# Kernel tuning notes

Hardware: AMD Instinct MI355X
Metric: run time of the kernel (lower is better)

The kernel has to match this reference:

```python
import jax, jax.numpy as jnp
import numpy as np

N_NODES = 50000
N_EDGES = 1600000
D = 64


def setup_inputs() -> dict:
    key = jax.random.key(0)
    ks = jax.random.split(key, 7)
    scale = 1.0 / np.sqrt(2 * D)  # keep activations sane through relu stack
    x = jax.random.normal(ks[0], (N_NODES, D), dtype=jnp.float32)
    edge_index = jax.random.randint(ks[1], (2, N_EDGES), 0, N_NODES, dtype=jnp.int32)
    edge_weight = jax.random.uniform(ks[2], (N_EDGES,), dtype=jnp.float32)
    W1 = jax.random.normal(ks[3], (D, 2 * D), dtype=jnp.float32) * scale
    b1 = jax.random.normal(ks[4], (D,), dtype=jnp.float32) * 0.01
    W2 = jax.random.normal(ks[5], (D, 2 * D), dtype=jnp.float32) * scale
    b2 = jax.random.normal(ks[6], (D,), dtype=jnp.float32) * 0.01
    return {"x": x, "edge_index": edge_index, "edge_weight": edge_weight,
            "W1": W1, "b1": b1, "W2": W2, "b2": b2}


def _sage_conv(x, src, dst, edge_weight, W, b):
    # gather neighbor features, weight, scatter-mean onto src nodes
    m = x[dst] * edge_weight[:, None]                      # [E, d]
    agg_sum = jax.ops.segment_sum(m, src, num_segments=x.shape[0])
    cnt = jax.ops.segment_sum(jnp.ones_like(edge_weight), src,
                              num_segments=x.shape[0])
    agg = agg_sum / jnp.maximum(cnt, 1.0)[:, None]          # scatter 'mean'
    h = jnp.concatenate([x, agg], axis=1)                   # [N, 2d]
    return h @ W.T + b


def reference(x, edge_index, edge_weight, W1, b1, W2, b2):
    src, dst = edge_index[0], edge_index[1]
    h = jax.nn.relu(_sage_conv(x, src, dst, edge_weight, W1, b1))
    h = jax.nn.relu(_sage_conv(h, src, dst, edge_weight, W2, b2))
    return h
```

## Files before the change

### kernel.cpp

```cpp
#include <hip/hip_runtime.h>

#define NN 50000
#define NE 1600000
#define DD 64
#define NPB 196
#define NBKT 256
#define CHUNK 2500
#define NBLK 640
#define SLOT 24
#define SSTR 25
#define S1CAP 1024
#define SPCAP 512
#define ELLW 72

typedef __attribute__((ext_vector_type(8))) short bf16x8;
typedef __attribute__((ext_vector_type(4))) float f32x4;
typedef __attribute__((ext_vector_type(2))) float f32x2;

static __device__ __forceinline__ unsigned short f2bf(float f) {
    unsigned int u = __float_as_uint(f);
    unsigned int r = (u + 0x7FFFu + ((u >> 16) & 1u)) >> 16;
    return (unsigned short)r;
}
static __device__ __forceinline__ float bf2f(unsigned short h) {
    return __uint_as_float((unsigned int)h << 16);
}
static __device__ __forceinline__ unsigned int pk_fp8x4(float a, float b, float c, float d) {
    unsigned int p = __builtin_amdgcn_cvt_pk_fp8_f32(a, b, 0u, false);
    p = __builtin_amdgcn_cvt_pk_fp8_f32(c, d, p, true);
    return p;
}

__global__ __launch_bounds__(256) void prep_bin(
    const int* __restrict__ ei, const float* __restrict__ ew,
    int* __restrict__ gcur, int* __restrict__ gspillc,
    int2* __restrict__ buf1, int2* __restrict__ spill,
    const float* __restrict__ x, ushort* __restrict__ xb,
    unsigned int* __restrict__ xf8,
    const float* __restrict__ W1, const float* __restrict__ W2,
    ushort* __restrict__ W1b, ushort* __restrict__ W2b)
{
    __shared__ int2 slot[NBKT * SSTR];
    __shared__ int  lcnt[NBKT];
    __shared__ int  lbase[NBKT];
    int tid = threadIdx.x;
    int blk = blockIdx.x;

    if (blk >= NBLK) {
        int pb = blk - NBLK;
        if (pb < 3125) {
            int i = pb * 256 + tid;
            float4 v = ((const float4*)x)[i];
            ushort4 o;
            o.x = f2bf(v.x); o.y = f2bf(v.y); o.z = f2bf(v.z); o.w = f2bf(v.w);
            ((ushort4*)xb)[i] = o;
            xf8[i] = pk_fp8x4(v.x, v.y, v.z, v.w);
        } else {
            int i = (pb - 3125) * 256 + tid;
            const float* src = (i < 2048) ? W1 : W2;
            ushort* dst = (i < 2048) ? W1b : W2b;
            int j = i & 2047;
            float4 v = ((const float4*)src)[j];
            ushort4 o;
            o.x = f2bf(v.x); o.y = f2bf(v.y); o.z = f2bf(v.z); o.w = f2bf(v.w);
            ((ushort4*)dst)[j] = o;
        }
        return;
    }

    int shard = blk & 7;
    for (int b = tid; b < NBKT; b += 256) lcnt[b] = 0;
    __syncthreads();

    int g0 = blk * (CHUNK / 4);
    const int4*   s4 = (const int4*)ei;
    const int4*   d4 = ((const int4*)ei) + NE / 4;
    const float4* w4 = (const float4*)ew;
    for (int it = 0; it < 3; ++it) {
        int idx = it * 256 + tid;
        if (idx >= CHUNK / 4) break;
        int4 sv = s4[g0 + idx];
        int4 dv = d4[g0 + idx];
        float4 wv = w4[g0 + idx];
#pragma unroll
        for (int k = 0; k < 4; ++k) {
            int s = (k == 0) ? sv.x : (k == 1) ? sv.y : (k == 2) ? sv.z : sv.w;
            int d = (k == 0) ? dv.x : (k == 1) ? dv.y : (k == 2) ? dv.z : dv.w;
            float w = (k == 0) ? wv.x : (k == 1) ? wv.y : (k == 2) ? wv.z : wv.w;
            int bkt = s / NPB;
            int sloc = s - bkt * NPB;
            int2 rec = make_int2(d | ((int)f2bf(w) << 16), sloc);
            int pos = atomicAdd(&lcnt[bkt], 1);
            if (pos < SLOT) {
                slot[bkt * SSTR + pos] = rec;
            } else {
                int sp = atomicAdd(&gspillc[bkt], 1);
                if (sp < SPCAP) spill[bkt * SPCAP + sp] = rec;
            }
        }
    }
    __syncthreads();

    {
        int b = tid;
        int n = lcnt[b]; if (n > SLOT) n = SLOT;
        lcnt[b] = n;
        lbase[b] = (n > 0) ? atomicAdd(&gcur[b * 8 + shard], n) : 0;
    }
    __syncthreads();

    int wave = tid >> 6, lane = tid & 63;
    int b0 = wave * 64;
    int vcnt = lcnt[b0 + lane];
    int vbase = lbase[b0 + lane];
#pragma unroll 8
    for (int j = 0; j < 64; ++j) {
        int n = __shfl(vcnt, j);
        int base = __shfl(vbase, j);
        int b = b0 + j;
        if (lane < n) {
            int2 rec = slot[b * SSTR + lane];
            int p = base + lane;
            if (p < S1CAP) {
                buf1[((size_t)b * 8 + shard) * S1CAP + p] = rec;
            } else {
                int sp = atomicAdd(&gspillc[b], 1);
                if (sp < SPCAP) spill[b * SPCAP + sp] = rec;
            }
        }
    }
}

__global__ __launch_bounds__(1024) void build_ell(
    const int* __restrict__ gcur, const int2* __restrict__ buf1,
    const int* __restrict__ gspillc, const int2* __restrict__ spill,
    unsigned int* __restrict__ csr, int* __restrict__ cnt)
{
    __shared__ int cur[NPB];
    int tid = threadIdx.x, bkt = blockIdx.x;

    if (tid < NPB) cur[tid] = 0;
    __syncthreads();

    for (int sh = 0; sh < 9; ++sh) {
        int n; const int2* rp;
        if (sh < 8) {
            n = gcur[bkt * 8 + sh]; if (n > S1CAP) n = S1CAP;
            rp = buf1 + ((size_t)bkt * 8 + sh) * S1CAP;
        } else {
            n = gspillc[bkt]; if (n > SPCAP) n = SPCAP;
            rp = spill + (size_t)bkt * SPCAP;
        }
        for (int i = tid; i < n; i += 1024) {
            int2 r = rp[i];
            int pos = atomicAdd(&cur[r.y], 1);
            if (pos < ELLW)
                csr[((size_t)(bkt * NPB + r.y)) * ELLW + pos] = (unsigned int)r.x;
        }
    }
    __syncthreads();

    if (tid < NPB) {
        int node = bkt * NPB + tid;
        if (node < NN) {
            int deg = cur[tid];
            cnt[node] = deg;
            int c = deg < ELLW ? deg : ELLW;
            int c4 = (c + 3) & ~3;
            for (int p = c; p < c4; ++p)
                csr[(size_t)node * ELLW + p] = 0u;
        }
    }
}

__global__ __launch_bounds__(1024) void fused_layer(
    const ushort* __restrict__ Xb,
    const unsigned int* __restrict__ f8,
    const int* __restrict__ cnt, const unsigned int* __restrict__ csr,
    const ushort* __restrict__ Wb, const float* __restrict__ bias,
    float* __restrict__ out, ushort* __restrict__ outb,
    unsigned char* __restrict__ outf8)
{
    __shared__ ushort xL[16][72];
    __shared__ ushort aggL[16][72];
    int tid = threadIdx.x;
    int wave = tid >> 6, lane = tid & 63;
    int g = lane >> 4, l16 = lane & 15;
    int base = blockIdx.x * 16;
    int node = base + wave;

    if (lane < 16)
        *(ushort4*)&xL[wave][l16 * 4] =
            *(const ushort4*)&Xb[(size_t)node * DD + l16 * 4];

    int nd = cnt[node];
    int n = nd < ELLW ? nd : ELLW;
    int n4 = (n + 3) & ~3;
    const unsigned int* __restrict__ rp = csr + (size_t)node * ELLW;
    float a0 = 0.f, a1 = 0.f, a2 = 0.f, a3 = 0.f;

    int i = 0;
    for (; i + 16 <= n4; i += 16) {
        uint4 r = *(const uint4*)(rp + i + g * 4);
        unsigned int v0 = f8[(r.x & 0xFFFF) * 16 + l16];
        unsigned int v1 = f8[(r.y & 0xFFFF) * 16 + l16];
        unsigned int v2 = f8[(r.z & 0xFFFF) * 16 + l16];
        unsigned int v3 = f8[(r.w & 0xFFFF) * 16 + l16];
        float w0 = bf2f((unsigned short)(r.x >> 16));
        float w1 = bf2f((unsigned short)(r.y >> 16));
        float w2 = bf2f((unsigned short)(r.z >> 16));
        float w3 = bf2f((unsigned short)(r.w >> 16));
        f32x2 lo, hi;
        lo = __builtin_amdgcn_cvt_pk_f32_fp8(v0, false);
        hi = __builtin_amdgcn_cvt_pk_f32_fp8(v0, true);
        a0 += w0 * lo.x; a1 += w0 * lo.y; a2 += w0 * hi.x; a3 += w0 * hi.y;
        lo = __builtin_amdgcn_cvt_pk_f32_fp8(v1, false);
        hi = __builtin_amdgcn_cvt_pk_f32_fp8(v1, true);
        a0 += w1 * lo.x; a1 += w1 * lo.y; a2 += w1 * hi.x; a3 += w1 * hi.y;
        lo = __builtin_amdgcn_cvt_pk_f32_fp8(v2, false);
        hi = __builtin_amdgcn_cvt_pk_f32_fp8(v2, true);
        a0 += w2 * lo.x; a1 += w2 * lo.y; a2 += w2 * hi.x; a3 += w2 * hi.y;
        lo = __builtin_amdgcn_cvt_pk_f32_fp8(v3, false);
        hi = __builtin_amdgcn_cvt_pk_f32_fp8(v3, true);
        a0 += w3 * lo.x; a1 += w3 * lo.y; a2 += w3 * hi.x; a3 += w3 * hi.y;
    }
    for (; i < n4; i += 4) {
        uint4 r = *(const uint4*)(rp + i);
        unsigned int e = (g == 0) ? r.x : (g == 1) ? r.y : (g == 2) ? r.z : r.w;
        unsigned int v = f8[(e & 0xFFFF) * 16 + l16];
        float w = bf2f((unsigned short)(e >> 16));
        f32x2 lo = __builtin_amdgcn_cvt_pk_f32_fp8(v, false);
        f32x2 hi = __builtin_amdgcn_cvt_pk_f32_fp8(v, true);
        a0 += w * lo.x; a1 += w * lo.y; a2 += w * hi.x; a3 += w * hi.y;
    }

    a0 += __shfl_xor(a0, 16); a0 += __shfl_xor(a0, 32);
    a1 += __shfl_xor(a1, 16); a1 += __shfl_xor(a1, 32);
    a2 += __shfl_xor(a2, 16); a2 += __shfl_xor(a2, 32);
    a3 += __shfl_xor(a3, 16); a3 += __shfl_xor(a3, 32);

    if (lane < 16) {
        float dm = (float)(nd > 1 ? nd : 1);
        ushort4 o;
        o.x = f2bf(a0 / dm); o.y = f2bf(a1 / dm);
        o.z = f2bf(a2 / dm); o.w = f2bf(a3 / dm);
        *(ushort4*)&aggL[wave][l16 * 4] = o;
    }
    __syncthreads();

    if (wave < 4) {
        f32x4 acc = (f32x4){0.f, 0.f, 0.f, 0.f};
#pragma unroll
        for (int ki = 0; ki < 4; ++ki) {
            const ushort* ap = (ki < 2) ? &xL[l16][ki * 32 + g * 8]
                                        : &aggL[l16][(ki - 2) * 32 + g * 8];
            bf16x8 af = *(const bf16x8*)ap;
            bf16x8 bfrag = *(const bf16x8*)&Wb[(size_t)(wave * 16 + l16) * 128 + ki * 32 + g * 8];
            acc = __builtin_amdgcn_mfma_f32_16x16x32_bf16(af, bfrag, acc, 0, 0, 0);
        }
        int col = wave * 16 + l16;
        float bv = bias[col];
#pragma unroll
        for (int r = 0; r < 4; ++r) {
            int grow = base + g * 4 + r;
            float v = fmaxf(acc[r] + bv, 0.f);
            if (out)  out[(size_t)grow * DD + col] = v;
            if (outb) outb[(size_t)grow * DD + col] = f2bf(v);
            if (outf8) {
                unsigned int p = __builtin_amdgcn_cvt_pk_fp8_f32(v, v, 0u, false);
                outf8[(size_t)grow * DD + col] = (unsigned char)(p & 0xFFu);
            }
        }
    }
}

extern "C" void kernel_launch(void* const* d_in, const int* in_sizes, int n_in,
                              void* d_out, int out_size, void* d_ws, size_t ws_size,
                              hipStream_t stream)
{
    const float* x  = (const float*)d_in[0];
    const int*   ei = (const int*)d_in[1];
    const float* ew = (const float*)d_in[2];
    const float* W1 = (const float*)d_in[3];
    const float* b1 = (const float*)d_in[4];
    const float* W2 = (const float*)d_in[5];
    const float* b2 = (const float*)d_in[6];
    float* out = (float*)d_out;

    char* ws = (char*)d_ws;
    int*          gcur    = (int*)ws;
    int*          gspillc = (int*)(ws + 8192);
    int2*         buf1    = (int2*)(ws + 16384);
    int2*         spill   = (int2*)(ws + 16793600);
    unsigned int* csr     = (unsigned int*)(ws + 17842176);
    int*          cnt     = (int*)(ws + 32292864);
    ushort*       xb      = (ushort*)(ws + 32493568);
    ushort*       h1b     = (ushort*)(ws + 38893568);
    ushort*       W1b     = (ushort*)(ws + 45293568);
    ushort*       W2b     = (ushort*)(ws + 45309952);
    unsigned int* xf8     = (unsigned int*)(ws + 45326336);
    unsigned char* h1f8   = (unsigned char*)(ws + 48526336);

    hipMemsetAsync(gcur, 0, 9216, stream);

    prep_bin<<<NBLK + 3141, 256, 0, stream>>>(ei, ew, gcur, gspillc, buf1, spill,
                                              x, xb, xf8, W1, W2, W1b, W2b);
    build_ell<<<NBKT, 1024, 0, stream>>>(gcur, buf1, gspillc, spill, csr, cnt);

    fused_layer<<<NN / 16, 1024, 0, stream>>>(xb, xf8, cnt, csr, W1b, b1,
                                              nullptr, h1b, h1f8);
    fused_layer<<<NN / 16, 1024, 0, stream>>>(h1b, (const unsigned int*)h1f8,
                                              cnt, csr, W2b, b2, out, nullptr, nullptr);
}
```

Baseline: 195.9 us.

## Build ELL adjacency directly with global atomics, dropping two-pass bucket binning

Replaces the two-kernel bucketed binning (shared-memory slots, sharded staging buffers, spill, then per-bucket ELL build) with a single scatter kernel. Each edge does a global atomicAdd on its source node's count and writes the packed record straight into the ELL row. This removes one kernel launch and a round trip through the staging buffers. The cost is 1.6M global atomics spread over 50K counters, uncoalesced writes, and masked tail handling in the aggregation loop instead of zero padding.

```diff
diff --git a/kernel.cpp b/kernel.cpp
--- a/kernel.cpp
+++ b/kernel.cpp
@@ -3,15 +3,8 @@
 #define NN 50000
 #define NE 1600000
 #define DD 64
-#define NPB 196
-#define NBKT 256
-#define CHUNK 2500
-#define NBLK 640
-#define SLOT 24
-#define SSTR 25
-#define S1CAP 1024
-#define SPCAP 512
 #define ELLW 72
+#define EBLK 1563
 
 typedef __attribute__((ext_vector_type(8))) short bf16x8;
 typedef __attribute__((ext_vector_type(4))) float f32x4;
@@ -31,23 +24,19 @@
     return p;
 }
 
-__global__ __launch_bounds__(256) void prep_bin(
+__global__ __launch_bounds__(256) void prep_scatter(
     const int* __restrict__ ei, const float* __restrict__ ew,
-    int* __restrict__ gcur, int* __restrict__ gspillc,
-    int2* __restrict__ buf1, int2* __restrict__ spill,
+    int* __restrict__ cnt, unsigned int* __restrict__ csr,
     const float* __restrict__ x, ushort* __restrict__ xb,
     unsigned int* __restrict__ xf8,
     const float* __restrict__ W1, const float* __restrict__ W2,
     ushort* __restrict__ W1b, ushort* __restrict__ W2b)
 {
-    __shared__ int2 slot[NBKT * SSTR];
-    __shared__ int  lcnt[NBKT];
-    __shared__ int  lbase[NBKT];
     int tid = threadIdx.x;
     int blk = blockIdx.x;
 
-    if (blk >= NBLK) {
-        int pb = blk - NBLK;
+    if (blk >= EBLK) {
+        int pb = blk - EBLK;
         if (pb < 3125) {
             int i = pb * 256 + tid;
             float4 v = ((const float4*)x)[i];
@@ -68,108 +57,23 @@
         return;
     }
 
-    int shard = blk & 7;
-    for (int b = tid; b < NBKT; b += 256) lcnt[b] = 0;
-    __syncthreads();
-
-    int g0 = blk * (CHUNK / 4);
+    int idx = blk * 256 + tid;
+    if (idx >= NE / 4) return;
     const int4*   s4 = (const int4*)ei;
     const int4*   d4 = ((const int4*)ei) + NE / 4;
     const float4* w4 = (const float4*)ew;
-    for (int it = 0; it < 3; ++it) {
-        int idx = it * 256 + tid;
-        if (idx >= CHUNK / 4) break;
-        int4 sv = s4[g0 + idx];
-        int4 dv = d4[g0 + idx];
-        float4 wv = w4[g0 + idx];
+    int4 sv = s4[idx];
+    int4 dv = d4[idx];
+    float4 wv = w4[idx];
 #pragma unroll
-        for (int k = 0; k < 4; ++k) {
-            int s = (k == 0) ? sv.x : (k == 1) ? sv.y : (k == 2) ? sv.z : sv.w;
-            int d = (k == 0) ? dv.x : (k == 1) ? dv.y : (k == 2) ? dv.z : dv.w;
-            float w = (k == 0) ? wv.x : (k == 1) ? wv.y : (k == 2) ? wv.z : wv.w;
-            int bkt = s / NPB;
-            int sloc = s - bkt * NPB;
-            int2 rec = make_int2(d | ((int)f2bf(w) << 16), sloc);
-            int pos = atomicAdd(&lcnt[bkt], 1);
-            if (pos < SLOT) {
-                slot[bkt * SSTR + pos] = rec;
-            } else {
-                int sp = atomicAdd(&gspillc[bkt], 1);
-                if (sp < SPCAP) spill[bkt * SPCAP + sp] = rec;
-            }
-        }
-    }
-    __syncthreads();
-
-    {
-        int b = tid;
-        int n = lcnt[b]; if (n > SLOT) n = SLOT;
-        lcnt[b] = n;
-        lbase[b] = (n > 0) ? atomicAdd(&gcur[b * 8 + shard], n) : 0;
-    }
-    __syncthreads();
-
-    int wave = tid >> 6, lane = tid & 63;
-    int b0 = wave * 64;
-    int vcnt = lcnt[b0 + lane];
-    int vbase = lbase[b0 + lane];
-#pragma unroll 8
-    for (int j = 0; j < 64; ++j) {
-        int n = __shfl(vcnt, j);
-        int base = __shfl(vbase, j);
-        int b = b0 + j;
-        if (lane < n) {
-            int2 rec = slot[b * SSTR + lane];
-            int p = base + lane;
-            if (p < S1CAP) {
-                buf1[((size_t)b * 8 + shard) * S1CAP + p] = rec;
-            } else {
-                int sp = atomicAdd(&gspillc[b], 1);
-                if (sp < SPCAP) spill[b * SPCAP + sp] = rec;
-            }
-        }
-    }
-}
-
-__global__ __launch_bounds__(1024) void build_ell(
-    const int* __restrict__ gcur, const int2* __restrict__ buf1,
-    const int* __restrict__ gspillc, const int2* __restrict__ spill,
-    unsigned int* __restrict__ csr, int* __restrict__ cnt)
-{
-    __shared__ int cur[NPB];
-    int tid = threadIdx.x, bkt = blockIdx.x;
-
-    if (tid < NPB) cur[tid] = 0;
-    __syncthreads();
-
-    for (int sh = 0; sh < 9; ++sh) {
-        int n; const int2* rp;
-        if (sh < 8) {
-            n = gcur[bkt * 8 + sh]; if (n > S1CAP) n = S1CAP;
-            rp = buf1 + ((size_t)bkt * 8 + sh) * S1CAP;
-        } else {
-            n = gspillc[bkt]; if (n > SPCAP) n = SPCAP;
-            rp = spill + (size_t)bkt * SPCAP;
-        }
-        for (int i = tid; i < n; i += 1024) {
-            int2 r = rp[i];
-            int pos = atomicAdd(&cur[r.y], 1);
-            if (pos < ELLW)
-                csr[((size_t)(bkt * NPB + r.y)) * ELLW + pos] = (unsigned int)r.x;
-        }
-    }
-    __syncthreads();
-
-    if (tid < NPB) {
-        int node = bkt * NPB + tid;
-        if (node < NN) {
-            int deg = cur[tid];
-            cnt[node] = deg;
-            int c = deg < ELLW ? deg : ELLW;
-            int c4 = (c + 3) & ~3;
-            for (int p = c; p < c4; ++p)
-                csr[(size_t)node * ELLW + p] = 0u;
-        }
+    for (int k = 0; k < 4; ++k) {
+        int s   = (k == 0) ? sv.x : (k == 1) ? sv.y : (k == 2) ? sv.z : sv.w;
+        int d   = (k == 0) ? dv.x : (k == 1) ? dv.y : (k == 2) ? dv.z : dv.w;
+        float w = (k == 0) ? wv.x : (k == 1) ? wv.y : (k == 2) ? wv.z : wv.w;
+        int pos = atomicAdd(&cnt[s], 1);
+        if (pos < ELLW)
+            csr[(size_t)s * ELLW + pos] =
+                (unsigned int)d | ((unsigned int)f2bf(w) << 16);
     }
 }
 
@@ -195,12 +99,11 @@
 
     int nd = cnt[node];
     int n = nd < ELLW ? nd : ELLW;
-    int n4 = (n + 3) & ~3;
     const unsigned int* __restrict__ rp = csr + (size_t)node * ELLW;
     float a0 = 0.f, a1 = 0.f, a2 = 0.f, a3 = 0.f;
 
     int i = 0;
-    for (; i + 16 <= n4; i += 16) {
+    for (; i + 16 <= n; i += 16) {
         uint4 r = *(const uint4*)(rp + i + g * 4);
         unsigned int v0 = f8[(r.x & 0xFFFF) * 16 + l16];
         unsigned int v1 = f8[(r.y & 0xFFFF) * 16 + l16];
@@ -224,9 +127,10 @@
         hi = __builtin_amdgcn_cvt_pk_f32_fp8(v3, true);
         a0 += w3 * lo.x; a1 += w3 * lo.y; a2 += w3 * hi.x; a3 += w3 * hi.y;
     }
-    for (; i < n4; i += 4) {
+    for (; i < n; i += 4) {
         uint4 r = *(const uint4*)(rp + i);
         unsigned int e = (g == 0) ? r.x : (g == 1) ? r.y : (g == 2) ? r.z : r.w;
+        if (i + g >= n) e = 0u;
         unsigned int v = f8[(e & 0xFFFF) * 16 + l16];
         float w = bf2f((unsigned short)(e >> 16));
         f32x2 lo = __builtin_amdgcn_cvt_pk_f32_fp8(v, false);
@@ -288,24 +192,19 @@
     float* out = (float*)d_out;
 
     char* ws = (char*)d_ws;
-    int*          gcur    = (int*)ws;
-    int*          gspillc = (int*)(ws + 8192);
-    int2*         buf1    = (int2*)(ws + 16384);
-    int2*         spill   = (int2*)(ws + 16793600);
-    unsigned int* csr     = (unsigned int*)(ws + 17842176);
-    int*          cnt     = (int*)(ws + 32292864);
-    ushort*       xb      = (ushort*)(ws + 32493568);
-    ushort*       h1b     = (ushort*)(ws + 38893568);
-    ushort*       W1b     = (ushort*)(ws + 45293568);
-    ushort*       W2b     = (ushort*)(ws + 45309952);
-    unsigned int* xf8     = (unsigned int*)(ws + 45326336);
-    unsigned char* h1f8   = (unsigned char*)(ws + 48526336);
-
-    hipMemsetAsync(gcur, 0, 9216, stream);
-
-    prep_bin<<<NBLK + 3141, 256, 0, stream>>>(ei, ew, gcur, gspillc, buf1, spill,
-                                              x, xb, xf8, W1, W2, W1b, W2b);
-    build_ell<<<NBKT, 1024, 0, stream>>>(gcur, buf1, gspillc, spill, csr, cnt);
+    int*          cnt  = (int*)ws;
+    unsigned int* csr  = (unsigned int*)(ws + 200704);
+    ushort*       xb   = (ushort*)(ws + 14600704);
+    ushort*       h1b  = (ushort*)(ws + 21000704);
+    ushort*       W1b  = (ushort*)(ws + 27400704);
+    ushort*       W2b  = (ushort*)(ws + 27417088);
+    unsigned int* xf8  = (unsigned int*)(ws + 27433472);
+    unsigned char* h1f8 = (unsigned char*)(ws + 30633472);
+
+    hipMemsetAsync(cnt, 0, 200704, stream);
+
+    prep_scatter<<<EBLK + 3141, 256, 0, stream>>>(ei, ew, cnt, csr,
+                                                  x, xb, xf8, W1, W2, W1b, W2b);
 
     fused_layer<<<NN / 16, 1024, 0, stream>>>(xb, xf8, cnt, csr, W1b, b1,
                                               nullptr, h1b, h1f8);
```

After: 309.5 us. 1.58x slower.
